# Optimization experiments

Hardware: AMD Instinct MI355X
Metric: run time of the kernel (lower is better)

## Reference

```python
import jax, jax.numpy as jnp
import numpy as np

NUM_HEADS = 8
NEG_MASK = -1000.0  # original code masks with -1000, not -inf


def setup_inputs() -> dict:
    key = jax.random.key(0)
    ks = jax.random.split(key, 12)
    B, S, D = 4, 2048, 512
    HID, OUT = 512, 512
    dh = D // NUM_HEADS      # 64, per-head input dim
    eh = HID // NUM_HEADS    # 64, per-head hidden dim
    w = 0.02
    return {
        "q": jax.random.normal(ks[0], (B, S, D), dtype=jnp.float32),
        "k": jax.random.normal(ks[1], (B, S, D), dtype=jnp.float32),
        "v": jax.random.normal(ks[2], (B, S, D), dtype=jnp.float32),
        # Linear weights stored as [in, out] (transpose of torch convention)
        "Wq": jax.random.normal(ks[3], (dh, eh), dtype=jnp.float32) * w,
        "bq": jax.random.normal(ks[4], (eh,), dtype=jnp.float32) * w,
        "Wk": jax.random.normal(ks[5], (dh, eh), dtype=jnp.float32) * w,
        "bk": jax.random.normal(ks[6], (eh,), dtype=jnp.float32) * w,
        "Wv": jax.random.normal(ks[7], (dh, eh), dtype=jnp.float32) * w,
        "bv": jax.random.normal(ks[8], (eh,), dtype=jnp.float32) * w,
        "Wo": jax.random.normal(ks[9], (HID, OUT), dtype=jnp.float32) * w,
        "bo": jax.random.normal(ks[10], (OUT,), dtype=jnp.float32) * w,
        "valid_lens": jnp.maximum(jax.random.randint(ks[11], (B,), 0, S), 1),
        "max_len": S,
    }


def reference(q, k, v, Wq, bq, Wk, bk, Wv, bv, Wo, bo, valid_lens, max_len):
    B, S, D = q.shape
    H = NUM_HEADS
    # split into heads: [B, S, H, dh]; note the SAME projection weights are
    # shared across heads (as in the original module)
    qh = q.reshape(B, S, H, D // H)
    kh = k.reshape(B, S, H, D // H)
    vh = v.reshape(B, S, H, D // H)
    qp = jnp.einsum('bshd,de->bshe', qh, Wq) + bq  # [B,S,H,eh]
    kp = jnp.einsum('bshd,de->bshe', kh, Wk) + bk
    vp = jnp.einsum('bshd,de->bshe', vh, Wv) + bv
    scale = 1.0 / jnp.sqrt(jnp.asarray(qp.shape[-1], qp.dtype))
    scores = jnp.einsum('bshe,bthe->bhst', qp, kp) * scale  # [B,H,S,S]
    # key-padding mask: positions j >= valid_len get -1000 (original semantics)
    key_mask = jnp.arange(S)[None, :] < valid_lens[:, None]  # [B,S]
    scores = jnp.where(key_mask[:, None, None, :], scores, NEG_MASK)
    attn = jax.nn.softmax(scores, axis=-1)
    ctx = jnp.einsum('bhst,bthe->bshe', attn, vp).reshape(B, S, -1)  # head-major concat
    return jnp.einsum('bse,eo->bso', ctx, Wo) + bo
```

## Files before the change

### kernel.cpp

```cpp
#include <hip/hip_runtime.h>

#define S_LEN 2048
#define D_MODEL 512

typedef __attribute__((ext_vector_type(8))) short s8v;
typedef __attribute__((ext_vector_type(4))) float f4v;
typedef __attribute__((ext_vector_type(4))) short s4v;
typedef __attribute__((ext_vector_type(4))) int   i4v;
typedef __attribute__((ext_vector_type(2))) int   i2v;

#define MFMA __builtin_amdgcn_mfma_f32_16x16x32_bf16

__device__ inline short f2bf(float x) {
    union { float f; unsigned u; } v; v.f = x;
    unsigned r = v.u + 0x7fffu + ((v.u >> 16) & 1u);
    return (short)(r >> 16);
}
__device__ inline unsigned pack_bf2_trunc(float a, float b) {
    unsigned ua = __builtin_bit_cast(unsigned, a);
    unsigned ub = __builtin_bit_cast(unsigned, b);
    return (ua >> 16) | (ub & 0xffff0000u);
}

template <int C>
__device__ inline float dppf(float x) {
    int i = __builtin_bit_cast(int, x);
    i = __builtin_amdgcn_update_dpp(0, i, C, 0xF, 0xF, true);
    return __builtin_bit_cast(float, i);
}
__device__ inline float rowsum16(float x) {
    x += dppf<0xB1>(x);
    x += dppf<0x4E>(x);
    x += dppf<0x141>(x);
    x += dppf<0x140>(x);
    return x;
}

typedef const __attribute__((address_space(1))) void* gptr_t;
typedef __attribute__((address_space(3))) void* sptr_t;
__device__ inline void gload16(const void* g, void* s) {
    __builtin_amdgcn_global_load_lds((gptr_t)g, (sptr_t)s, 16, 0, 0);
}

__global__ __launch_bounds__(256) void proj_kernel(
    const float* __restrict__ q, const float* __restrict__ k, const float* __restrict__ v,
    const float* __restrict__ Wq, const float* __restrict__ Wk, const float* __restrict__ Wv,
    const float* __restrict__ bq, const float* __restrict__ bk, const float* __restrict__ bv,
    const float* __restrict__ Wo, short* __restrict__ WoT,
    short* __restrict__ qp, short* __restrict__ kfrag, short* __restrict__ vfrag)
{
    __shared__ short sm[128 * 64];

    if (blockIdx.z == 12) {
        const int idx = blockIdx.y * 16 + blockIdx.x;
        if (idx >= 64) return;
        const int bi = (idx >> 3) * 64;
        const int bj = (idx & 7) * 64;
        const int c = threadIdx.x & 63, rr = threadIdx.x >> 6;
        short* t = sm;
#pragma unroll
        for (int r = 0; r < 16; r++) {
            int i = r * 4 + rr;
            t[c * 65 + i] = f2bf(Wo[(size_t)(bi + i) * 512 + bj + c]);
        }
        __syncthreads();
#pragma unroll
        for (int r = 0; r < 16; r++) {
            int o = r * 4 + rr;
            WoT[(size_t)(bj + o) * 512 + bi + c] = t[o * 65 + c];
        }
        return;
    }

    const int t = blockIdx.z >> 2;
    const int b = blockIdx.z & 3;
    const int h = blockIdx.y;
    const int qt = blockIdx.x;
    const int w = threadIdx.x >> 6, lane = threadIdx.x & 63;
    const int l = lane & 15, qd = lane >> 4;

    const float* X    = (t == 0) ? q  : (t == 1) ? k  : v;
    const float* Wp   = (t == 0) ? Wq : (t == 1) ? Wk : Wv;
    const float* bias = (t == 0) ? bq : (t == 1) ? bk : bv;

    {
        const int d = threadIdx.x >> 2, c4 = threadIdx.x & 3;
        const float* src = Wp + d * 64 + c4 * 16;
        f4v x0 = *(const f4v*)(src);
        f4v x1 = *(const f4v*)(src + 4);
        f4v x2 = *(const f4v*)(src + 8);
        f4v x3 = *(const f4v*)(src + 12);
        float xs[16] = {x0[0],x0[1],x0[2],x0[3], x1[0],x1[1],x1[2],x1[3],
                        x2[0],x2[1],x2[2],x2[3], x3[0],x3[1],x3[2],x3[3]};
#pragma unroll
        for (int j = 0; j < 16; j++) {
            int e = c4 * 16 + j;
            int sidx = (e * 64 + d) ^ (((e >> 2) & 7) << 3);
            sm[sidx] = f2bf(xs[j]);
        }
    }
    __syncthreads();

    const int s0 = qt * 128 + w * 32;

    s8v a[2][2];
#pragma unroll
    for (int mt = 0; mt < 2; mt++)
#pragma unroll
        for (int kk = 0; kk < 2; kk++) {
            const float* p = X + (size_t)(b * S_LEN + s0 + mt * 16 + l) * 512 + h * 64 + kk * 32 + qd * 8;
            f4v x0 = *(const f4v*)p;
            f4v x1 = *(const f4v*)(p + 4);
            s8v fr;
            fr[0] = f2bf(x0[0]); fr[1] = f2bf(x0[1]); fr[2] = f2bf(x0[2]); fr[3] = f2bf(x0[3]);
            fr[4] = f2bf(x1[0]); fr[5] = f2bf(x1[1]); fr[6] = f2bf(x1[2]); fr[7] = f2bf(x1[3]);
            a[mt][kk] = fr;
        }
    s8v wf[4][2];
#pragma unroll
    for (int nt = 0; nt < 4; nt++) {
        int wrow = (t < 2) ? (4 * l + nt) : (nt * 16 + l);
        int key = ((wrow >> 2) & 7) << 3;
#pragma unroll
        for (int kk = 0; kk < 2; kk++)
            wf[nt][kk] = *(const s8v*)(sm + ((wrow * 64 + kk * 32 + qd * 8) ^ key));
    }

    const f4v fz = {0.f, 0.f, 0.f, 0.f};
    f4v acc[2][4];
#pragma unroll
    for (int mt = 0; mt < 2; mt++)
#pragma unroll
        for (int nt = 0; nt < 4; nt++) acc[mt][nt] = fz;

#pragma unroll
    for (int kk = 0; kk < 2; kk++)
#pragma unroll
        for (int nt = 0; nt < 4; nt++)
#pragma unroll
            for (int mt = 0; mt < 2; mt++)
                acc[mt][nt] = MFMA(a[mt][kk], wf[nt][kk], acc[mt][nt], 0, 0, 0);

    const float SC = 0.125f * 1.442695041f;

    if (t == 0) {
        float bbs[4];
#pragma unroll
        for (int nt = 0; nt < 4; nt++) bbs[nt] = bias[4 * l + nt];
#pragma unroll
        for (int mt = 0; mt < 2; mt++)
#pragma unroll
            for (int r = 0; r < 4; r++) {
                int s = s0 + mt * 16 + qd * 4 + r;
                s4v pk;
#pragma unroll
                for (int nt = 0; nt < 4; nt++)
                    pk[nt] = f2bf((acc[mt][nt][r] + bbs[nt]) * SC);
                *(s4v*)(qp + ((size_t)(b * 8 + h) * S_LEN + s) * 64 + 4 * l) = pk;
            }
        return;
    }

    __syncthreads();

    if (t == 1) {
        float bbs[4];
#pragma unroll
        for (int nt = 0; nt < 4; nt++) bbs[nt] = bias[4 * l + nt];
#pragma unroll
        for (int mt = 0; mt < 2; mt++)
#pragma unroll
            for (int r = 0; r < 4; r++) {
                int sl = w * 32 + mt * 16 + qd * 4 + r;
                s4v pk;
#pragma unroll
                for (int nt = 0; nt < 4; nt++) pk[nt] = f2bf(acc[mt][nt][r] + bbs[nt]);
                int sidx = (sl * 64 + 4 * l) ^ (((sl >> 2) & 7) << 3);
                *(s4v*)(sm + sidx) = pk;
            }
    } else {
#pragma unroll
        for (int nt = 0; nt < 4; nt++) {
            float bb = bias[nt * 16 + l];
            int e = nt * 16 + l;
            int key = ((e >> 2) & 7) << 3;
#pragma unroll
            for (int mt = 0; mt < 2; mt++) {
                s4v pk;
#pragma unroll
                for (int r = 0; r < 4; r++) pk[r] = f2bf(acc[mt][nt][r] + bb);
                int sidx = (e * 128 + w * 32 + mt * 16 + qd * 4) ^ key;
                *(s4v*)(sm + sidx) = pk;
            }
        }
    }
    __syncthreads();

    short* dst = (t == 1) ? kfrag : vfrag;
    const size_t obase0 = ((size_t)(b * 8 + h) * 32 + qt * 2) * 4096;
    const int f = threadIdx.x & 63, cp = threadIdx.x >> 6;
    const int fl = f & 15, fq = f >> 4;
#pragma unroll
    for (int tt = 0; tt < 2; tt++)
#pragma unroll
        for (int ci = 0; ci < 2; ci++) {
            int c = cp + ci * 4;
            int n2 = c >> 1, kk = c & 1;
            int sidx;
            if (t == 1) {
                int sl = tt * 64 + 4 * fl + n2;
                sidx = (sl * 64 + kk * 32 + fq * 8) ^ (((sl >> 2) & 7) << 3);
            } else {
                int e = 4 * fl + n2;
                sidx = (e * 128 + tt * 64 + kk * 32 + fq * 8) ^ (((e >> 2) & 7) << 3);
            }
            s8v x = *(const s8v*)(sm + sidx);
            *(s8v*)(dst + obase0 + tt * 4096 + c * 512 + f * 8) = x;
        }
}

__global__ __launch_bounds__(256, 2) void attn_kernel(
    const short* __restrict__ qp, const short* __restrict__ kfrag,
    const short* __restrict__ vfrag,
    const int* __restrict__ valid_lens, short* __restrict__ ctx)
{
    __shared__ alignas(16) short kbuf[2][8192];
    __shared__ alignas(16) short lP[4][32 * 72];

    const int gid = blockIdx.x;
    const int h  = gid & 7;
    int b        = (gid >> 3) & 3;
    const int qt = gid >> 5;
    b ^= 3 * ((gid >> 8) & 1);
    const int w = threadIdx.x >> 6, lane = threadIdx.x & 63;
    const int l = lane & 15, qd = lane >> 4;
    const int vlen = valid_lens[b];
    const int nt2 = (vlen + 127) >> 7;

    const int bh = b * 8 + h;
    const short* Qs = qp + (size_t)bh * S_LEN * 64;
    const short* Kf = kfrag + (size_t)bh * 32 * 4096;
    const short* Vf = vfrag + (size_t)bh * 32 * 4096;

    const int s0 = qt * 128 + w * 32;
    s8v qf[2][2];
#pragma unroll
    for (int mt = 0; mt < 2; mt++)
#pragma unroll
        for (int kk = 0; kk < 2; kk++)
            qf[mt][kk] = *(const s8v*)(Qs + (size_t)(s0 + mt * 16 + l) * 64 + kk * 32 + qd * 8);

    const f4v fz = {0.f, 0.f, 0.f, 0.f};
    f4v O[2][4];
    float lsum[2][4];
#pragma unroll
    for (int mt = 0; mt < 2; mt++)
#pragma unroll
        for (int r = 0; r < 4; r++) lsum[mt][r] = 0.f;
#pragma unroll
    for (int mt = 0; mt < 2; mt++)
#pragma unroll
        for (int ne = 0; ne < 4; ne++) O[mt][ne] = fz;

    short* lPw = lP[w];
    const int toff = threadIdx.x * 8;

#pragma unroll
    for (int r = 0; r < 4; r++)
        gload16(Kf + r * 2048 + toff, &kbuf[0][r * 2048 + toff]);
    __syncthreads();

    for (int j = 0; j < nt2; j++) {
        const int cur = j & 1;
        if (j + 1 < nt2) {
            const short* Ks = Kf + (size_t)(j + 1) * 8192;
#pragma unroll
            for (int r = 0; r < 4; r++)
                gload16(Ks + r * 2048 + toff, &kbuf[cur ^ 1][r * 2048 + toff]);
        }

#pragma unroll
        for (int st = 0; st < 2; st++) {
            const int kb = 2 * j + st;

            const short* Vb = Vf + (size_t)kb * 4096 + lane * 8;
            s8v vf[4][2];
#pragma unroll
            for (int ne = 0; ne < 4; ne++)
#pragma unroll
                for (int kk = 0; kk < 2; kk++)
                    vf[ne][kk] = *(const s8v*)(Vb + (ne * 2 + kk) * 512);

            const short* Kb = &kbuf[cur][st * 4096 + lane * 8];
            s8v kf[4][2];
#pragma unroll
            for (int nt = 0; nt < 4; nt++)
#pragma unroll
                for (int kk = 0; kk < 2; kk++)
                    kf[nt][kk] = *(const s8v*)(Kb + (nt * 2 + kk) * 512);

            f4v sf[2][4];
#pragma unroll
            for (int mt = 0; mt < 2; mt++)
#pragma unroll
                for (int nt = 0; nt < 4; nt++) sf[mt][nt] = fz;
            __builtin_amdgcn_s_setprio(1);
#pragma unroll
            for (int nt = 0; nt < 4; nt++)
#pragma unroll
                for (int mt = 0; mt < 2; mt++) {
                    sf[mt][nt] = MFMA(qf[mt][0], kf[nt][0], sf[mt][nt], 0, 0, 0);
                    sf[mt][nt] = MFMA(qf[mt][1], kf[nt][1], sf[mt][nt], 0, 0, 0);
                }
            __builtin_amdgcn_s_setprio(0);

            if (j == nt2 - 1) {
                int rem = vlen - kb * 64;
                if (rem < 64) {
#pragma unroll
                    for (int nt = 0; nt < 4; nt++)
                        if (4 * l + nt >= rem) {
#pragma unroll
                            for (int mt = 0; mt < 2; mt++)
#pragma unroll
                                for (int r = 0; r < 4; r++) sf[mt][nt][r] = -1e30f;
                        }
                }
            }

#pragma unroll
            for (int mt = 0; mt < 2; mt++)
#pragma unroll
                for (int r = 0; r < 4; r++) {
                    float p0 = __builtin_amdgcn_exp2f(sf[mt][0][r]);
                    float p1 = __builtin_amdgcn_exp2f(sf[mt][1][r]);
                    float p2 = __builtin_amdgcn_exp2f(sf[mt][2][r]);
                    float p3 = __builtin_amdgcn_exp2f(sf[mt][3][r]);
                    lsum[mt][r] += (p0 + p1) + (p2 + p3);
                    i2v pk;
                    pk[0] = (int)pack_bf2_trunc(p0, p1);
                    pk[1] = (int)pack_bf2_trunc(p2, p3);
                    *(i2v*)(lPw + (mt * 16 + qd * 4 + r) * 72 + 4 * l) = pk;
                }

            s8v pa[2][2];
#pragma unroll
            for (int mt = 0; mt < 2; mt++)
#pragma unroll
                for (int kk = 0; kk < 2; kk++)
                    pa[mt][kk] = *(const s8v*)(lPw + (mt * 16 + l) * 72 + kk * 32 + qd * 8);
            __builtin_amdgcn_s_setprio(1);
#pragma unroll
            for (int ne = 0; ne < 4; ne++)
#pragma unroll
                for (int mt = 0; mt < 2; mt++) {
                    O[mt][ne] = MFMA(pa[mt][0], vf[ne][0], O[mt][ne], 0, 0, 0);
                    O[mt][ne] = MFMA(pa[mt][1], vf[ne][1], O[mt][ne], 0, 0, 0);
                }
            __builtin_amdgcn_s_setprio(0);
        }

        __syncthreads();
    }

#pragma unroll
    for (int mt = 0; mt < 2; mt++)
#pragma unroll
        for (int r = 0; r < 4; r++) {
            float inv = 1.0f / rowsum16(lsum[mt][r]);
            int s = s0 + mt * 16 + qd * 4 + r;
            s4v pk;
#pragma unroll
            for (int ne = 0; ne < 4; ne++) pk[ne] = f2bf(O[mt][ne][r] * inv);
            *(s4v*)(ctx + ((size_t)(b * S_LEN + s)) * 512 + h * 64 + 4 * l) = pk;
        }
}

__global__ __launch_bounds__(256) void outproj_kernel(
    const short* __restrict__ ctx, const short* __restrict__ WoT,
    const float* __restrict__ bo, float* __restrict__ out)
{
    __shared__ short lB[64 * 520];
    __shared__ short lA[128 * 40];

    const int rb = blockIdx.x * 128;
    const int nb = blockIdx.y * 64;
    const int w = threadIdx.x >> 6, lane = threadIdx.x & 63;
    const int l = lane & 15, qd = lane >> 4;

    {
        int n = threadIdx.x >> 2, c0 = threadIdx.x & 3;
#pragma unroll
        for (int i = 0; i < 16; i++) {
            int g = i * 4 + c0;
            i4v x = *(const i4v*)(WoT + (size_t)(nb + n) * 512 + g * 8);
            *(i4v*)(lB + n * 520 + g * 8) = x;
        }
    }
    __syncthreads();

    const f4v fz = {0.f, 0.f, 0.f, 0.f};
    f4v acc[2][4];
#pragma unroll
    for (int mt = 0; mt < 2; mt++)
#pragma unroll
        for (int nt = 0; nt < 4; nt++) acc[mt][nt] = fz;

    for (int ko = 0; ko < 16; ko++) {
        {
            int r = threadIdx.x >> 1, hp = threadIdx.x & 1;
            const short* src = ctx + (size_t)(rb + r) * 512 + ko * 32 + hp * 16;
            i4v x0 = *(const i4v*)src;
            i4v x1 = *(const i4v*)(src + 8);
            *(i4v*)(lA + r * 40 + hp * 16) = x0;
            *(i4v*)(lA + r * 40 + hp * 16 + 8) = x1;
        }
        __syncthreads();
        s8v af[2];
#pragma unroll
        for (int mt = 0; mt < 2; mt++)
            af[mt] = *(const s8v*)(lA + (w * 32 + mt * 16 + l) * 40 + qd * 8);
#pragma unroll
        for (int nt = 0; nt < 4; nt++) {
            s8v bfr = *(const s8v*)(lB + (nt * 16 + l) * 520 + ko * 32 + qd * 8);
#pragma unroll
            for (int mt = 0; mt < 2; mt++)
                acc[mt][nt] = MFMA(af[mt], bfr, acc[mt][nt], 0, 0, 0);
        }
        __syncthreads();
    }

#pragma unroll
    for (int nt = 0; nt < 4; nt++) {
        float bias = bo[nb + nt * 16 + l];
#pragma unroll
        for (int mt = 0; mt < 2; mt++)
#pragma unroll
            for (int r = 0; r < 4; r++) {
                int row = rb + w * 32 + mt * 16 + qd * 4 + r;
                out[(size_t)row * 512 + nb + nt * 16 + l] = acc[mt][nt][r] + bias;
            }
    }
}

extern "C" void kernel_launch(void* const* d_in, const int* in_sizes, int n_in,
                              void* d_out, int out_size, void* d_ws, size_t ws_size,
                              hipStream_t stream)
{
    const float* q  = (const float*)d_in[0];
    const float* k  = (const float*)d_in[1];
    const float* v  = (const float*)d_in[2];
    const float* Wq = (const float*)d_in[3];
    const float* bq = (const float*)d_in[4];
    const float* Wk = (const float*)d_in[5];
    const float* bk = (const float*)d_in[6];
    const float* Wv = (const float*)d_in[7];
    const float* bv = (const float*)d_in[8];
    const float* Wo = (const float*)d_in[9];
    const float* bo = (const float*)d_in[10];
    const int*   vl = (const int*)d_in[11];
    float* out = (float*)d_out;

    char* ws = (char*)d_ws;
    const size_t SL = (size_t)4 * 8 * S_LEN * 64 * sizeof(short);
    short* qp    = (short*)(ws);
    short* ctx   = (short*)(ws + SL);
    short* kfrag = (short*)(ws + 2 * SL);
    short* vfrag = (short*)(ws + 3 * SL);
    short* WoT   = (short*)(ws + 4 * SL);

    proj_kernel<<<dim3(16, 8, 13), 256, 0, stream>>>(q, k, v, Wq, Wk, Wv,
                                                     bq, bk, bv, Wo, WoT,
                                                     qp, kfrag, vfrag);
    attn_kernel<<<512, 256, 0, stream>>>(qp, kfrag, vfrag, vl, ctx);
    outproj_kernel<<<dim3(64, 8), 256, 0, stream>>>(ctx, WoT, bo, out);
}
```

Baseline: 165.9 us.

## Replace LDS-staged K tiles with register double-buffered K/V prefetch in attention

The attention kernel no longer stages K tiles through shared memory with global_load_lds and per-iteration __syncthreads. Each wave instead loads its K and V fragments directly from global memory into two register buffers, prefetching the next 64-key tile while computing the current one. The aim is to remove block-wide barriers and LDS traffic for K. In exchange, register pressure rises, and the launch bound no longer requests two blocks per CU, which may reduce occupancy. Each wave also now issues its own global K loads instead of sharing one LDS copy across the block.

Result: slower. 185.3 us (+11.7%).

```diff
diff --git a/kernel.cpp b/kernel.cpp
--- a/kernel.cpp
+++ b/kernel.cpp
@@ -34,12 +34,6 @@
     x += dppf<0x141>(x);
     x += dppf<0x140>(x);
     return x;
-}
-
-typedef const __attribute__((address_space(1))) void* gptr_t;
-typedef __attribute__((address_space(3))) void* sptr_t;
-__device__ inline void gload16(const void* g, void* s) {
-    __builtin_amdgcn_global_load_lds((gptr_t)g, (sptr_t)s, 16, 0, 0);
 }
 
 __global__ __launch_bounds__(256) void proj_kernel(
@@ -219,12 +213,11 @@
         }
 }
 
-__global__ __launch_bounds__(256, 2) void attn_kernel(
+__global__ __launch_bounds__(256) void attn_kernel(
     const short* __restrict__ qp, const short* __restrict__ kfrag,
     const short* __restrict__ vfrag,
     const int* __restrict__ valid_lens, short* __restrict__ ctx)
 {
-    __shared__ alignas(16) short kbuf[2][8192];
     __shared__ alignas(16) short lP[4][32 * 72];
 
     const int gid = blockIdx.x;
@@ -235,12 +228,12 @@
     const int w = threadIdx.x >> 6, lane = threadIdx.x & 63;
     const int l = lane & 15, qd = lane >> 4;
     const int vlen = valid_lens[b];
-    const int nt2 = (vlen + 127) >> 7;
+    const int ntiles = (vlen + 63) >> 6;
 
     const int bh = b * 8 + h;
     const short* Qs = qp + (size_t)bh * S_LEN * 64;
-    const short* Kf = kfrag + (size_t)bh * 32 * 4096;
-    const short* Vf = vfrag + (size_t)bh * 32 * 4096;
+    const short* Kf = kfrag + (size_t)bh * 32 * 4096 + lane * 8;
+    const short* Vf = vfrag + (size_t)bh * 32 * 4096 + lane * 8;
 
     const int s0 = qt * 128 + w * 32;
     s8v qf[2][2];
@@ -263,104 +256,87 @@
         for (int ne = 0; ne < 4; ne++) O[mt][ne] = fz;
 
     short* lPw = lP[w];
-    const int toff = threadIdx.x * 8;
-
-#pragma unroll
-    for (int r = 0; r < 4; r++)
-        gload16(Kf + r * 2048 + toff, &kbuf[0][r * 2048 + toff]);
-    __syncthreads();
-
-    for (int j = 0; j < nt2; j++) {
-        const int cur = j & 1;
-        if (j + 1 < nt2) {
-            const short* Ks = Kf + (size_t)(j + 1) * 8192;
-#pragma unroll
-            for (int r = 0; r < 4; r++)
-                gload16(Ks + r * 2048 + toff, &kbuf[cur ^ 1][r * 2048 + toff]);
-        }
-
-#pragma unroll
-        for (int st = 0; st < 2; st++) {
-            const int kb = 2 * j + st;
-
-            const short* Vb = Vf + (size_t)kb * 4096 + lane * 8;
-            s8v vf[4][2];
-#pragma unroll
-            for (int ne = 0; ne < 4; ne++)
-#pragma unroll
-                for (int kk = 0; kk < 2; kk++)
-                    vf[ne][kk] = *(const s8v*)(Vb + (ne * 2 + kk) * 512);
-
-            const short* Kb = &kbuf[cur][st * 4096 + lane * 8];
-            s8v kf[4][2];
+
+    s8v kA[4][2], vA[4][2], kB[4][2], vB[4][2];
+
+    auto LOAD = [&](s8v (&kf)[4][2], s8v (&vf)[4][2], int kb) {
+        const short* Kb = Kf + (size_t)kb * 4096;
+        const short* Vb = Vf + (size_t)kb * 4096;
+#pragma unroll
+        for (int c = 0; c < 8; c++) {
+            kf[c >> 1][c & 1] = *(const s8v*)(Kb + c * 512);
+            vf[c >> 1][c & 1] = *(const s8v*)(Vb + c * 512);
+        }
+    };
+
+    auto BODY = [&](const s8v (&kf)[4][2], const s8v (&vf)[4][2], int kb) {
+        f4v sf[2][4];
+#pragma unroll
+        for (int mt = 0; mt < 2; mt++)
+#pragma unroll
+            for (int nt = 0; nt < 4; nt++) sf[mt][nt] = fz;
+        __builtin_amdgcn_s_setprio(1);
+#pragma unroll
+        for (int nt = 0; nt < 4; nt++)
+#pragma unroll
+            for (int mt = 0; mt < 2; mt++) {
+                sf[mt][nt] = MFMA(qf[mt][0], kf[nt][0], sf[mt][nt], 0, 0, 0);
+                sf[mt][nt] = MFMA(qf[mt][1], kf[nt][1], sf[mt][nt], 0, 0, 0);
+            }
+        __builtin_amdgcn_s_setprio(0);
+
+        if (kb == ntiles - 1 && (vlen & 63)) {
+            int rem = vlen - kb * 64;
 #pragma unroll
             for (int nt = 0; nt < 4; nt++)
-#pragma unroll
-                for (int kk = 0; kk < 2; kk++)
-                    kf[nt][kk] = *(const s8v*)(Kb + (nt * 2 + kk) * 512);
-
-            f4v sf[2][4];
-#pragma unroll
-            for (int mt = 0; mt < 2; mt++)
-#pragma unroll
-                for (int nt = 0; nt < 4; nt++) sf[mt][nt] = fz;
-            __builtin_amdgcn_s_setprio(1);
-#pragma unroll
-            for (int nt = 0; nt < 4; nt++)
-#pragma unroll
-                for (int mt = 0; mt < 2; mt++) {
-                    sf[mt][nt] = MFMA(qf[mt][0], kf[nt][0], sf[mt][nt], 0, 0, 0);
-                    sf[mt][nt] = MFMA(qf[mt][1], kf[nt][1], sf[mt][nt], 0, 0, 0);
+                if (4 * l + nt >= rem) {
+#pragma unroll
+                    for (int mt = 0; mt < 2; mt++)
+#pragma unroll
+                        for (int r = 0; r < 4; r++) sf[mt][nt][r] = -1e30f;
                 }
-            __builtin_amdgcn_s_setprio(0);
-
-            if (j == nt2 - 1) {
-                int rem = vlen - kb * 64;
-                if (rem < 64) {
-#pragma unroll
-                    for (int nt = 0; nt < 4; nt++)
-                        if (4 * l + nt >= rem) {
-#pragma unroll
-                            for (int mt = 0; mt < 2; mt++)
-#pragma unroll
-                                for (int r = 0; r < 4; r++) sf[mt][nt][r] = -1e30f;
-                        }
-                }
-            }
-
-#pragma unroll
-            for (int mt = 0; mt < 2; mt++)
-#pragma unroll
-                for (int r = 0; r < 4; r++) {
-                    float p0 = __builtin_amdgcn_exp2f(sf[mt][0][r]);
-                    float p1 = __builtin_amdgcn_exp2f(sf[mt][1][r]);
-                    float p2 = __builtin_amdgcn_exp2f(sf[mt][2][r]);
-                    float p3 = __builtin_amdgcn_exp2f(sf[mt][3][r]);
-                    lsum[mt][r] += (p0 + p1) + (p2 + p3);
-                    i2v pk;
-                    pk[0] = (int)pack_bf2_trunc(p0, p1);
-                    pk[1] = (int)pack_bf2_trunc(p2, p3);
-                    *(i2v*)(lPw + (mt * 16 + qd * 4 + r) * 72 + 4 * l) = pk;
-                }
-
-            s8v pa[2][2];
-#pragma unroll
-            for (int mt = 0; mt < 2; mt++)
-#pragma unroll
-                for (int kk = 0; kk < 2; kk++)
-                    pa[mt][kk] = *(const s8v*)(lPw + (mt * 16 + l) * 72 + kk * 32 + qd * 8);
-            __builtin_amdgcn_s_setprio(1);
-#pragma unroll
-            for (int ne = 0; ne < 4; ne++)
-#pragma unroll
-                for (int mt = 0; mt < 2; mt++) {
-                    O[mt][ne] = MFMA(pa[mt][0], vf[ne][0], O[mt][ne], 0, 0, 0);
-                    O[mt][ne] = MFMA(pa[mt][1], vf[ne][1], O[mt][ne], 0, 0, 0);
-                }
-            __builtin_amdgcn_s_setprio(0);
-        }
-
-        __syncthreads();
+        }
+
+#pragma unroll
+        for (int mt = 0; mt < 2; mt++)
+#pragma unroll
+            for (int r = 0; r < 4; r++) {
+                float p0 = __builtin_amdgcn_exp2f(sf[mt][0][r]);
+                float p1 = __builtin_amdgcn_exp2f(sf[mt][1][r]);
+                float p2 = __builtin_amdgcn_exp2f(sf[mt][2][r]);
+                float p3 = __builtin_amdgcn_exp2f(sf[mt][3][r]);
+                lsum[mt][r] += (p0 + p1) + (p2 + p3);
+                i2v pk;
+                pk[0] = (int)pack_bf2_trunc(p0, p1);
+                pk[1] = (int)pack_bf2_trunc(p2, p3);
+                *(i2v*)(lPw + (mt * 16 + qd * 4 + r) * 72 + 4 * l) = pk;
+            }
+
+        s8v pa[2][2];
+#pragma unroll
+        for (int mt = 0; mt < 2; mt++)
+#pragma unroll
+            for (int kk = 0; kk < 2; kk++)
+                pa[mt][kk] = *(const s8v*)(lPw + (mt * 16 + l) * 72 + kk * 32 + qd * 8);
+        __builtin_amdgcn_s_setprio(1);
+#pragma unroll
+        for (int ne = 0; ne < 4; ne++)
+#pragma unroll
+            for (int mt = 0; mt < 2; mt++) {
+                O[mt][ne] = MFMA(pa[mt][0], vf[ne][0], O[mt][ne], 0, 0, 0);
+                O[mt][ne] = MFMA(pa[mt][1], vf[ne][1], O[mt][ne], 0, 0, 0);
+            }
+        __builtin_amdgcn_s_setprio(0);
+    };
+
+    LOAD(kA, vA, 0);
+    for (int kb = 0; kb < ntiles; kb += 2) {
+        if (kb + 1 < ntiles) LOAD(kB, vB, kb + 1);
+        BODY(kA, vA, kb);
+        if (kb + 1 < ntiles) {
+            if (kb + 2 < ntiles) LOAD(kA, vA, kb + 2);
+            BODY(kB, vB, kb + 1);
+        }
     }
 
 #pragma unroll
```
